# Optimization experiments

Measured on AMD Instinct MI355X. Metric: run time of the kernel, lower is better.

## Reference

```python
import jax, jax.numpy as jnp
import numpy as np

S, B, C = 7, 2, 20
LAMBDA_COORD = 5.0
LAMBDA_NOOBJ = 0.5
EPS_WH = 1e-6
EPS_IOU = 1e-6
BATCH = 16384


def _iou_yolo(b1, b2):
    # b*: [..., 4] in (xc, yc, w, h) format
    b1x1 = b1[..., 0] - b1[..., 2] / 2
    b1y1 = b1[..., 1] - b1[..., 3] / 2
    b1x2 = b1[..., 0] + b1[..., 2] / 2
    b1y2 = b1[..., 1] + b1[..., 3] / 2
    b2x1 = b2[..., 0] - b2[..., 2] / 2
    b2y1 = b2[..., 1] - b2[..., 3] / 2
    b2x2 = b2[..., 0] + b2[..., 2] / 2
    b2y2 = b2[..., 1] + b2[..., 3] / 2
    iw = jnp.clip(jnp.minimum(b1x2, b2x2) - jnp.maximum(b1x1, b2x1), 0.0)
    ih = jnp.clip(jnp.minimum(b1y2, b2y2) - jnp.maximum(b1y1, b2y1), 0.0)
    inter = iw * ih
    a1 = jnp.abs((b1x2 - b1x1) * (b1y2 - b1y1))
    a2 = jnp.abs((b2x2 - b2x1) * (b2y2 - b2y1))
    return inter / (a1 + a2 - inter + EPS_IOU)


def setup_inputs() -> dict:
    key = jax.random.key(0)
    k1, k2, k3 = jax.random.split(key, 3)
    y_trues = jax.random.uniform(k1, (BATCH, S, S, 5 * B + C), dtype=jnp.float32)
    # conf1 channel must be exactly 1.0 for object cells (code checks == 1)
    obj = (jax.random.uniform(k3, (BATCH, S, S)) < 0.3).astype(jnp.float32)
    y_trues = y_trues.at[..., 4].set(obj)
    y_preds = jax.random.normal(k2, (BATCH, S, S, 5 * B + C), dtype=jnp.float32)
    return {"y_trues": y_trues, "y_preds": y_preds}


def reference(y_trues, y_preds):
    bs = y_trues.shape[0]
    yt = y_trues.reshape(bs, S * S, C + B * 5)
    yp = y_preds.reshape(bs, S * S, C + B * 5)

    obj = (yt[..., 4] == 1.0)            # [bs, S*S] bool
    objf = obj.astype(yt.dtype)
    noobjf = 1.0 - objf

    b = yt[..., 0:4]
    bhat1 = yp[..., 0:4]
    bhat2 = yp[..., 5:9]

    iou1 = _iou_yolo(b, bhat1)
    iou2 = _iou_yolo(b, bhat2)
    best1 = iou1 > iou2                  # [bs, S*S]

    bhat = jnp.where(best1[..., None], bhat1, bhat2)          # responsible box
    confhat = jnp.where(best1, yp[..., 4], yp[..., 9])

    # xy offset loss
    xy = (b[..., 0] - bhat[..., 0]) ** 2 + (b[..., 1] - bhat[..., 1]) ** 2
    xy_loss = LAMBDA_COORD * jnp.sum(objf * xy)

    # wh loss (sqrt targets, abs+eps on predictions)
    w_term = (jnp.sqrt(b[..., 2]) - jnp.sqrt(jnp.abs(bhat[..., 2] + EPS_WH))) ** 2
    h_term = (jnp.sqrt(b[..., 3]) - jnp.sqrt(jnp.abs(bhat[..., 3] + EPS_WH))) ** 2
    wh_loss = LAMBDA_COORD * jnp.sum(objf * (w_term + h_term))

    # object confidence loss (conf_i is 1 for obj cells)
    conf_loss = jnp.sum(objf * (yt[..., 4] - confhat) ** 2)

    # no-object confidence loss over both predicted boxes
    noobj_terms = (yt[..., 4:5] - yp[..., 4::5]) ** 2        # [bs, S*S, B]
    noobj_loss = LAMBDA_NOOBJ * jnp.sum(noobjf[..., None] * noobj_terms)

    # class loss
    cls = jnp.sum((yt[..., 10:] - yp[..., 10:]) ** 2, axis=-1)
    cls_loss = jnp.sum(objf * cls)

    total = xy_loss + wh_loss + conf_loss + noobj_loss + cls_loss
    return total / bs
```

## Files before the change

kernel.cpp:

```cpp
#include <hip/hip_runtime.h>

constexpr int   BATCH        = 16384;
constexpr int   CELLS        = 802816;
constexpr int   F            = 30;
constexpr int   CPT          = 64;
constexpr int   NTILES       = CELLS / CPT;
constexpr int   TILE_B       = CPT * F * 4;
constexpr int   GRID         = 512;
constexpr int   NWAVES       = GRID * 2;
constexpr float LAMBDA_COORD = 5.0f;
constexpr float LAMBDA_NOOBJ = 0.5f;
constexpr float EPS_WH       = 1e-6f;
constexpr float EPS_IOU      = 1e-6f;

__device__ __forceinline__ void load_lds16(const void* g, void* l) {
    __builtin_amdgcn_global_load_lds(
        (const __attribute__((address_space(1))) unsigned int*)g,
        (__attribute__((address_space(3))) unsigned int*)l,
        16, 0, 0);
}
__device__ __forceinline__ void load_lds4(const void* g, void* l) {
    __builtin_amdgcn_global_load_lds(
        (const __attribute__((address_space(1))) unsigned int*)g,
        (__attribute__((address_space(3))) unsigned int*)l,
        4, 0, 0);
}

__device__ __forceinline__ void stage_tile(const char* tg, const char* pg,
                                           char* lt, char* lp, int lane) {
#pragma unroll
    for (int j = 0; j < 7; ++j) {
        load_lds16(tg + j * 1024 + lane * 16, lt + j * 1024);
        load_lds16(pg + j * 1024 + lane * 16, lp + j * 1024);
    }
#pragma unroll
    for (int j = 0; j < 2; ++j) {
        load_lds4(tg + 7168 + j * 256 + lane * 4, lt + 7168 + j * 256);
        load_lds4(pg + 7168 + j * 256 + lane * 4, lp + 7168 + j * 256);
    }
}

__device__ __forceinline__ float iou_yolo(const float b0, const float b1,
                                          const float b2, const float b3,
                                          const float c0, const float c1,
                                          const float c2, const float c3) {
    float b1x1 = b0 - b2 * 0.5f;
    float b1y1 = b1 - b3 * 0.5f;
    float b1x2 = b0 + b2 * 0.5f;
    float b1y2 = b1 + b3 * 0.5f;
    float b2x1 = c0 - c2 * 0.5f;
    float b2y1 = c1 - c3 * 0.5f;
    float b2x2 = c0 + c2 * 0.5f;
    float b2y2 = c1 + c3 * 0.5f;
    float iw = fmaxf(fminf(b1x2, b2x2) - fmaxf(b1x1, b2x1), 0.0f);
    float ih = fmaxf(fminf(b1y2, b2y2) - fmaxf(b1y1, b2y1), 0.0f);
    float inter = iw * ih;
    float a1 = fabsf((b1x2 - b1x1) * (b1y2 - b1y1));
    float a2 = fabsf((b2x2 - b2x1) * (b2y2 - b2y1));
    return inter / (a1 + a2 - inter + EPS_IOU);
}

__global__ void __launch_bounds__(128)
yolo_loss_kernel(const float* __restrict__ yt_g,
                 const float* __restrict__ yp_g,
                 float* __restrict__ out) {
    __shared__ __align__(16) float lbuf[2][2][2][CPT * F];

    const int tid  = threadIdx.x;
    const int lane = tid & 63;
    const int wid  = tid >> 6;
    const int wgid = blockIdx.x * 2 + wid;

    int tile = wgid;
    stage_tile((const char*)yt_g + (size_t)tile * TILE_B,
               (const char*)yp_g + (size_t)tile * TILE_B,
               (char*)lbuf[wid][0][0], (char*)lbuf[wid][0][1], lane);

    float acc = 0.0f;
    int buf = 0;

    for (; tile < NTILES; tile += NWAVES) {
        const int next = tile + NWAVES;
        if (next < NTILES) {
            stage_tile((const char*)yt_g + (size_t)next * TILE_B,
                       (const char*)yp_g + (size_t)next * TILE_B,
                       (char*)lbuf[wid][buf ^ 1][0], (char*)lbuf[wid][buf ^ 1][1], lane);
            asm volatile("s_waitcnt vmcnt(18)" ::: "memory");
        } else {
            asm volatile("s_waitcnt vmcnt(0)" ::: "memory");
        }

        const float2* t2 = reinterpret_cast<const float2*>(&lbuf[wid][buf][0][lane * F]);
        const float2* p2 = reinterpret_cast<const float2*>(&lbuf[wid][buf][1][lane * F]);
        float t[F], p[F];
        {
            float2 v;
            v = t2[0]; t[0] = v.x; t[1] = v.y;
            v = t2[1]; t[2] = v.x; t[3] = v.y;
            v = t2[2]; t[4] = v.x;
#pragma unroll
            for (int k = 5; k < 15; ++k) { v = t2[k]; t[2 * k] = v.x; t[2 * k + 1] = v.y; }
        }
#pragma unroll
        for (int k = 0; k < 15; ++k) { float2 w = p2[k]; p[2 * k] = w.x; p[2 * k + 1] = w.y; }

        const float objf   = (t[4] == 1.0f) ? 1.0f : 0.0f;
        const float noobjf = 1.0f - objf;

        const float iou1 = iou_yolo(t[0], t[1], t[2], t[3], p[0], p[1], p[2], p[3]);
        const float iou2 = iou_yolo(t[0], t[1], t[2], t[3], p[5], p[6], p[7], p[8]);
        const bool  best1 = iou1 > iou2;

        const float bh0 = best1 ? p[0] : p[5];
        const float bh1 = best1 ? p[1] : p[6];
        const float bh2 = best1 ? p[2] : p[7];
        const float bh3 = best1 ? p[3] : p[8];
        const float confhat = best1 ? p[4] : p[9];

        const float dx = t[0] - bh0;
        const float dy = t[1] - bh1;
        const float xy = dx * dx + dy * dy;

        const float wt = sqrtf(t[2]) - sqrtf(fabsf(bh2 + EPS_WH));
        const float ht = sqrtf(t[3]) - sqrtf(fabsf(bh3 + EPS_WH));
        const float wh = wt * wt + ht * ht;

        const float dc = t[4] - confhat;

        float cls = 0.0f;
#pragma unroll
        for (int c = 10; c < F; ++c) {
            const float d = t[c] - p[c];
            cls += d * d;
        }
        float noobj = 0.0f;
#pragma unroll
        for (int c = 4; c < F; c += 5) {
            const float d = t[4] - p[c];
            noobj += d * d;
        }

        acc += objf * (LAMBDA_COORD * (xy + wh) + dc * dc + cls)
             + noobjf * (LAMBDA_NOOBJ * noobj);

        buf ^= 1;
    }

#pragma unroll
    for (int off = 32; off > 0; off >>= 1) acc += __shfl_down(acc, off);

    __shared__ float wsum[2];
    if (lane == 0) wsum[wid] = acc;
    __syncthreads();
    if (tid == 0) atomicAdd(out, (wsum[0] + wsum[1]) * (1.0f / (float)BATCH));
}

extern "C" void kernel_launch(void* const* d_in, const int* in_sizes, int n_in,
                              void* d_out, int out_size, void* d_ws, size_t ws_size,
                              hipStream_t stream) {
    const float* y_trues = (const float*)d_in[0];
    const float* y_preds = (const float*)d_in[1];
    float* out = (float*)d_out;

    hipMemsetAsync(out, 0, sizeof(float) * (size_t)out_size, stream);

    yolo_loss_kernel<<<GRID, 128, 0, stream>>>(y_trues, y_preds, out);
}
```

Baseline: 41.41 us.

## Stage tiles through registers instead of direct global-to-LDS loads, four waves per block

Replaces the global_load_lds double-buffered LDS staging with coalesced float2 register prefetch of the next tile, which is written into a single LDS buffer after compute finishes. Block size doubles to four waves per block with launch bounds allowing two blocks per CU, so more waves are resident to hide memory latency. The cost is 60 extra VGPRs per lane for the prefetch and a full wait for the loads before the LDS write-back, which removes the partial vmcnt overlap the old version had.

```diff
diff --git a/kernel.cpp b/kernel.cpp
--- a/kernel.cpp
+++ b/kernel.cpp
@@ -5,40 +5,14 @@
 constexpr int   F            = 30;
 constexpr int   CPT          = 64;
 constexpr int   NTILES       = CELLS / CPT;
-constexpr int   TILE_B       = CPT * F * 4;
+constexpr int   TFL2         = CPT * F / 2;
 constexpr int   GRID         = 512;
-constexpr int   NWAVES       = GRID * 2;
+constexpr int   WPB          = 4;
+constexpr int   NWAVES       = GRID * WPB;
 constexpr float LAMBDA_COORD = 5.0f;
 constexpr float LAMBDA_NOOBJ = 0.5f;
 constexpr float EPS_WH       = 1e-6f;
 constexpr float EPS_IOU      = 1e-6f;
-
-__device__ __forceinline__ void load_lds16(const void* g, void* l) {
-    __builtin_amdgcn_global_load_lds(
-        (const __attribute__((address_space(1))) unsigned int*)g,
-        (__attribute__((address_space(3))) unsigned int*)l,
-        16, 0, 0);
-}
-__device__ __forceinline__ void load_lds4(const void* g, void* l) {
-    __builtin_amdgcn_global_load_lds(
-        (const __attribute__((address_space(1))) unsigned int*)g,
-        (__attribute__((address_space(3))) unsigned int*)l,
-        4, 0, 0);
-}
-
-__device__ __forceinline__ void stage_tile(const char* tg, const char* pg,
-                                           char* lt, char* lp, int lane) {
-#pragma unroll
-    for (int j = 0; j < 7; ++j) {
-        load_lds16(tg + j * 1024 + lane * 16, lt + j * 1024);
-        load_lds16(pg + j * 1024 + lane * 16, lp + j * 1024);
-    }
-#pragma unroll
-    for (int j = 0; j < 2; ++j) {
-        load_lds4(tg + 7168 + j * 256 + lane * 4, lt + 7168 + j * 256);
-        load_lds4(pg + 7168 + j * 256 + lane * 4, lp + 7168 + j * 256);
-    }
-}
 
 __device__ __forceinline__ float iou_yolo(const float b0, const float b1,
                                           const float b2, const float b3,
@@ -60,38 +34,54 @@
     return inter / (a1 + a2 - inter + EPS_IOU);
 }
 
-__global__ void __launch_bounds__(128)
+__global__ void __launch_bounds__(256, 2)
 yolo_loss_kernel(const float* __restrict__ yt_g,
                  const float* __restrict__ yp_g,
                  float* __restrict__ out) {
-    __shared__ __align__(16) float lbuf[2][2][2][CPT * F];
+    __shared__ __align__(16) float lbuf[WPB][2][CPT * F];
 
     const int tid  = threadIdx.x;
     const int lane = tid & 63;
     const int wid  = tid >> 6;
-    const int wgid = blockIdx.x * 2 + wid;
+    const int wgid = blockIdx.x * WPB + wid;
+
+    const float2* tg2 = reinterpret_cast<const float2*>(yt_g);
+    const float2* pg2 = reinterpret_cast<const float2*>(yp_g);
+    float2* lt2 = reinterpret_cast<float2*>(lbuf[wid][0]);
+    float2* lp2 = reinterpret_cast<float2*>(lbuf[wid][1]);
+
+    float2 rt[15], rp[15];
 
     int tile = wgid;
-    stage_tile((const char*)yt_g + (size_t)tile * TILE_B,
-               (const char*)yp_g + (size_t)tile * TILE_B,
-               (char*)lbuf[wid][0][0], (char*)lbuf[wid][0][1], lane);
+    {
+        const size_t b2i = (size_t)tile * TFL2;
+#pragma unroll
+        for (int j = 0; j < 15; ++j) {
+            rt[j] = tg2[b2i + lane + 64 * j];
+            rp[j] = pg2[b2i + lane + 64 * j];
+        }
+#pragma unroll
+        for (int j = 0; j < 15; ++j) {
+            lt2[lane + 64 * j] = rt[j];
+            lp2[lane + 64 * j] = rp[j];
+        }
+    }
 
     float acc = 0.0f;
-    int buf = 0;
 
     for (; tile < NTILES; tile += NWAVES) {
         const int next = tile + NWAVES;
         if (next < NTILES) {
-            stage_tile((const char*)yt_g + (size_t)next * TILE_B,
-                       (const char*)yp_g + (size_t)next * TILE_B,
-                       (char*)lbuf[wid][buf ^ 1][0], (char*)lbuf[wid][buf ^ 1][1], lane);
-            asm volatile("s_waitcnt vmcnt(18)" ::: "memory");
-        } else {
-            asm volatile("s_waitcnt vmcnt(0)" ::: "memory");
+            const size_t b2i = (size_t)next * TFL2;
+#pragma unroll
+            for (int j = 0; j < 15; ++j) {
+                rt[j] = tg2[b2i + lane + 64 * j];
+                rp[j] = pg2[b2i + lane + 64 * j];
+            }
         }
 
-        const float2* t2 = reinterpret_cast<const float2*>(&lbuf[wid][buf][0][lane * F]);
-        const float2* p2 = reinterpret_cast<const float2*>(&lbuf[wid][buf][1][lane * F]);
+        const float2* t2 = reinterpret_cast<const float2*>(&lbuf[wid][0][lane * F]);
+        const float2* p2 = reinterpret_cast<const float2*>(&lbuf[wid][1][lane * F]);
         float t[F], p[F];
         {
             float2 v;
@@ -143,16 +133,29 @@
         acc += objf * (LAMBDA_COORD * (xy + wh) + dc * dc + cls)
              + noobjf * (LAMBDA_NOOBJ * noobj);
 
-        buf ^= 1;
+        if (next < NTILES) {
+            asm volatile("s_waitcnt lgkmcnt(0)" ::: "memory");
+            asm volatile("s_waitcnt vmcnt(0)" ::: "memory");
+#pragma unroll
+            for (int j = 0; j < 15; ++j) {
+                lt2[lane + 64 * j] = rt[j];
+                lp2[lane + 64 * j] = rp[j];
+            }
+        }
     }
 
 #pragma unroll
     for (int off = 32; off > 0; off >>= 1) acc += __shfl_down(acc, off);
 
-    __shared__ float wsum[2];
+    __shared__ float wsum[WPB];
     if (lane == 0) wsum[wid] = acc;
     __syncthreads();
-    if (tid == 0) atomicAdd(out, (wsum[0] + wsum[1]) * (1.0f / (float)BATCH));
+    if (tid == 0) {
+        float s = 0.0f;
+#pragma unroll
+        for (int w = 0; w < WPB; ++w) s += wsum[w];
+        atomicAdd(out, s * (1.0f / (float)BATCH));
+    }
 }
 
 extern "C" void kernel_launch(void* const* d_in, const int* in_sizes, int n_in,
@@ -164,5 +167,5 @@
 
     hipMemsetAsync(out, 0, sizeof(float) * (size_t)out_size, stream);
 
-    yolo_loss_kernel<<<GRID, 128, 0, stream>>>(y_trues, y_preds, out);
+    yolo_loss_kernel<<<GRID, 256, 0, stream>>>(y_trues, y_preds, out);
 }
```

New measurement: 37.96 us. 8.3% less time.
